# Performance work log

Measured on AMD Instinct MI355X. Metric: run time of the kernel, lower is better.

Reference implementation:

```python
import jax, jax.numpy as jnp
import numpy as np

D_MODEL = 2048
N_HEADS = 16
HEAD_DIM = D_MODEL // N_HEADS
D_FF = 8192


def setup_inputs() -> dict:
    key = jax.random.key(0)
    ks = jax.random.split(key, 16)
    s = 0.02
    inp = {
        'x': jax.random.normal(ks[0], (2, 2048, D_MODEL), dtype=jnp.float32),
        'Wq': jax.random.normal(ks[1], (D_MODEL, D_MODEL), jnp.float32) * s,
        'bq': jnp.zeros((D_MODEL,), jnp.float32),
        'Wk': jax.random.normal(ks[2], (D_MODEL, D_MODEL), jnp.float32) * s,
        'bk': jnp.zeros((D_MODEL,), jnp.float32),
        'Wv': jax.random.normal(ks[3], (D_MODEL, D_MODEL), jnp.float32) * s,
        'bv': jnp.zeros((D_MODEL,), jnp.float32),
        'Wo': jax.random.normal(ks[4], (D_MODEL, D_MODEL), jnp.float32) * s,
        'bo': jnp.zeros((D_MODEL,), jnp.float32),
        'rotary': jax.random.normal(ks[5], (1, 1, HEAD_DIM), jnp.float32) * s,
        'norm1_w': jnp.ones((D_MODEL,), jnp.float32),
        'norm2_w': jnp.ones((D_MODEL,), jnp.float32),
        'W1': jax.random.normal(ks[6], (2 * D_FF, D_MODEL), jnp.float32) * s,
        'b1': jnp.zeros((2 * D_FF,), jnp.float32),
        'W2': jax.random.normal(ks[7], (D_MODEL, D_FF), jnp.float32) * s,
        'b2': jnp.zeros((D_MODEL,), jnp.float32),
    }
    return inp


def _rmsnorm(x, w, eps=1e-8):
    return w * (x * jax.lax.rsqrt(jnp.mean(x * x, axis=-1, keepdims=True) + eps))


def reference(x, Wq, bq, Wk, bk, Wv, bv, Wo, bo, rotary, norm1_w, norm2_w, W1, b1, W2, b2):
    B, S, _ = x.shape
    # --- attention block ---
    h = _rmsnorm(x, norm1_w)
    q = (h @ Wq.T + bq).reshape(B, S, N_HEADS, HEAD_DIM)
    k = (h @ Wk.T + bk).reshape(B, S, N_HEADS, HEAD_DIM)
    v = (h @ Wv.T + bv).reshape(B, S, N_HEADS, HEAD_DIM)
    q = q + rotary  # (1,1,head_dim) broadcast over batch, seq, heads
    scores = jnp.einsum('bqhd,bkhd->bhqk', q, k) / jnp.sqrt(jnp.float32(HEAD_DIM))
    attn = jax.nn.softmax(scores, axis=-1)
    o = jnp.einsum('bhqk,bkhd->bqhd', attn, v).reshape(B, S, D_MODEL)
    x = x + (o @ Wo.T + bo)
    # --- SwiGLU FFN block ---
    h2 = _rmsnorm(x, norm2_w)
    g = h2 @ W1.T + b1
    x1, x2 = g[..., :D_FF], g[..., D_FF:]
    ff = (x1 * jax.nn.silu(x2)) @ W2.T + b2
    return x + ff
```

## Files before the change

### kernel.cpp

```cpp
#include <hip/hip_runtime.h>
#include <hip/hip_bf16.h>

#define D_MODEL 2048
#define N_HEADS 16
#define HEAD_DIM 128
#define D_FF 8192
#define BATCH 2
#define SEQ 2048
#define M_TOK (BATCH * SEQ)
#define QKV_LD 6144
#define QSCALE 0.12751744f

typedef __attribute__((ext_vector_type(8))) short short8;
typedef __attribute__((ext_vector_type(4))) short short4v;
typedef __attribute__((ext_vector_type(4))) float f32x4;
typedef __attribute__((ext_vector_type(16))) float f32x16;
typedef __attribute__((ext_vector_type(2))) unsigned int uint2v;
typedef __attribute__((ext_vector_type(4))) unsigned int uint4v;

__device__ __forceinline__ unsigned short f2b(float f) {
  __hip_bfloat16 h = __float2bfloat16(f);
  return *reinterpret_cast<unsigned short*>(&h);
}
__device__ __forceinline__ float b2f(unsigned short u) {
  unsigned int x = ((unsigned int)u) << 16;
  return __uint_as_float(x);
}

__device__ __forceinline__ void gload_lds16(const void* gsrc, void* ldst) {
  __builtin_amdgcn_global_load_lds(
      (const __attribute__((address_space(1))) void*)gsrc,
      (__attribute__((address_space(3))) void*)ldst, 16, 0, 0);
}

__device__ __forceinline__ f32x16 mfma32(short8 a, short8 b, f32x16 c) {
  return __builtin_amdgcn_mfma_f32_32x32x16_bf16(a, b, c, 0, 0, 0);
}
__device__ __forceinline__ unsigned int cvtpk(float lo, float hi) {
  unsigned int r;
  asm("v_cvt_pk_bf16_f32 %0, %1, %2" : "=v"(r) : "v"(lo), "v"(hi));
  return r;
}
__device__ __forceinline__ uint2v plswap(unsigned int a, unsigned int b) {
  return __builtin_amdgcn_permlane32_swap(a, b, false, false);
}

__global__ __launch_bounds__(256)
void cvt_all_kernel(const float* __restrict__ Wq, const float* __restrict__ Wk,
                    const float* __restrict__ Wv, const float* __restrict__ Wo,
                    const float* __restrict__ W2w,
                    unsigned short* __restrict__ wqkv,
                    unsigned short* __restrict__ wo,
                    unsigned short* __restrict__ w2) {
  const int NC = (D_MODEL * D_MODEL) / 8;
  const int TOT = 4 * NC + (D_MODEL * D_FF) / 8;
  int i = blockIdx.x * 256 + threadIdx.x;
  int stride = gridDim.x * 256;
  for (int c = i; c < TOT; c += stride) {
    const float* s;
    unsigned short* d;
    float sc = 1.0f;
    if (c < NC) { s = Wq + (size_t)c * 8; d = wqkv + (size_t)c * 8; sc = QSCALE; }
    else if (c < 2 * NC) { s = Wk + (size_t)(c - NC) * 8; d = wqkv + (size_t)c * 8; }
    else if (c < 3 * NC) { s = Wv + (size_t)(c - 2 * NC) * 8; d = wqkv + (size_t)c * 8; }
    else if (c < 4 * NC) { s = Wo + (size_t)(c - 3 * NC) * 8; d = wo + (size_t)(c - 3 * NC) * 8; }
    else { s = W2w + (size_t)(c - 4 * NC) * 8; d = w2 + (size_t)(c - 4 * NC) * 8; }
    const float4 a = *(const float4*)s;
    const float4 b = *(const float4*)(s + 4);
    short8 r;
    r[0] = f2b(a.x * sc); r[1] = f2b(a.y * sc);
    r[2] = f2b(a.z * sc); r[3] = f2b(a.w * sc);
    r[4] = f2b(b.x * sc); r[5] = f2b(b.y * sc);
    r[6] = f2b(b.z * sc); r[7] = f2b(b.w * sc);
    *(short8*)d = r;
  }
}

__global__ __launch_bounds__(256)
void cvt_w1p_kernel(const float* __restrict__ src,
                    unsigned short* __restrict__ dst) {
  int i = blockIdx.x * blockDim.x + threadIdx.x;
  int stride = gridDim.x * blockDim.x;
  const int total = 2 * D_FF * (D_MODEL / 8);
  for (int c = i; c < total; c += stride) {
    int rp = c >> 8, col8 = c & 255;
    int b = rp >> 6, half = (rp >> 5) & 1;
    int rs = half * D_FF + b * 32 + (rp & 31);
    const float* s = src + (size_t)rs * D_MODEL + col8 * 8;
    const float4 a = *(const float4*)s;
    const float4 bb = *(const float4*)(s + 4);
    short8 r;
    r[0] = f2b(a.x); r[1] = f2b(a.y); r[2] = f2b(a.z); r[3] = f2b(a.w);
    r[4] = f2b(bb.x); r[5] = f2b(bb.y); r[6] = f2b(bb.z); r[7] = f2b(bb.w);
    *(short8*)(dst + (size_t)c * 8) = r;
  }
}

__global__ void permb1_kernel(const float* __restrict__ b1,
                              float* __restrict__ b1p) {
  int i = blockIdx.x * 256 + threadIdx.x;
  int b = i >> 6, half = (i >> 5) & 1;
  b1p[i] = b1[half * D_FF + b * 32 + (i & 31)];
}

__global__ void biasqkv_kernel(const float* __restrict__ bq,
                               const float* __restrict__ bk,
                               const float* __restrict__ bv,
                               const float* __restrict__ rot,
                               float* __restrict__ outp) {
  int i = blockIdx.x * 256 + threadIdx.x;
  float v;
  if (i < 2048) v = (bq[i] + rot[i & (HEAD_DIM - 1)]) * QSCALE;
  else if (i < 4096) v = bk[i - 2048];
  else v = bv[i - 4096];
  outp[i] = v;
}

__global__ __launch_bounds__(256)
void rmsnorm_kernel(const float* __restrict__ x, const float* __restrict__ wv,
                    unsigned short* __restrict__ outp) {
  const int row = blockIdx.x;
  const float* xr = x + (size_t)row * D_MODEL;
  const int base = threadIdx.x * 8;
  float4 a = *(const float4*)(xr + base);
  float4 c = *(const float4*)(xr + base + 4);
  float ss = a.x * a.x + a.y * a.y + a.z * a.z + a.w * a.w +
             c.x * c.x + c.y * c.y + c.z * c.z + c.w * c.w;
#pragma unroll
  for (int m = 1; m < 64; m <<= 1) ss += __shfl_xor(ss, m);
  __shared__ float red[4];
  if ((threadIdx.x & 63) == 0) red[threadIdx.x >> 6] = ss;
  __syncthreads();
  float tot = red[0] + red[1] + red[2] + red[3];
  float sc = rsqrtf(tot * (1.0f / D_MODEL) + 1e-8f);
  float4 w0 = *(const float4*)(wv + base);
  float4 w1 = *(const float4*)(wv + base + 4);
  short8 r;
  r[0] = f2b(a.x * sc * w0.x); r[1] = f2b(a.y * sc * w0.y);
  r[2] = f2b(a.z * sc * w0.z); r[3] = f2b(a.w * sc * w0.w);
  r[4] = f2b(c.x * sc * w1.x); r[5] = f2b(c.y * sc * w1.y);
  r[6] = f2b(c.z * sc * w1.z); r[7] = f2b(c.w * sc * w1.w);
  *(short8*)(outp + (size_t)row * D_MODEL + base) = r;
}

template <int MODE>
__global__ __launch_bounds__(512, 2)
void gemm_p8(const unsigned short* __restrict__ A, int lda,
             const unsigned short* __restrict__ W, int ldw,
             const float* __restrict__ bias, void* __restrict__ outp,
             int N, int K, size_t out_zstride) {
  __shared__ unsigned short AL[2][2][128 * 64];
  __shared__ unsigned short BL[2][2][128 * 64];
  const int t = threadIdx.x;
  const int l = t & 63, w = t >> 6;
  const int wm = w >> 2, wn = w & 3;
  const int ln = l & 31, hi = l >> 5;
  const int m0 = blockIdx.y << 8, n0 = blockIdx.x << 8;
  const int koff = blockIdx.z * K;

  const int r0 = t >> 3;
  const int cb16 = (t & 7) * 16;
  const int sel = ((cb16 ^ ((r0 & 7) << 4)) >> 1);
  const unsigned short* Abase = A + (size_t)m0 * lda + koff;
  const unsigned short* Wbase = W + (size_t)n0 * ldw + koff;
  const int d0e = t * 8, d1e = (t + 512) * 8;

#define STAGE(XL, Xb, ld, dd, h, ktd)                                        \
  do {                                                                       \
    const unsigned short* s_ =                                               \
        (Xb) + (size_t)((h) * 128 + r0) * (ld) + (ktd) * 64 + sel;           \
    gload_lds16(s_, &XL[dd][h][d0e]);                                        \
    gload_lds16(s_ + (size_t)64 * (ld), &XL[dd][h][d1e]);                    \
  } while (0)

  const int swz = (ln & 7) << 4;
  const int hb = wn >> 1;
  const int browb = ((wn & 1) * 64 + ln) * 128;

  f32x16 acc[4][2] = {};
  short8 bf[2][4];

#define READB(dd)                                                            \
  do {                                                                       \
    const char* Bb_ = (const char*)&BL[dd][hb][0];                           \
    _Pragma("unroll") for (int cb_ = 0; cb_ < 2; cb_++)                      \
      _Pragma("unroll") for (int ks_ = 0; ks_ < 4; ks_++)                    \
        bf[cb_][ks_] = *(const short8*)(Bb_ + browb + cb_ * 4096 +           \
                                        ((ks_ * 32 + hi * 16) ^ swz));       \
  } while (0)

#define PHASE2(dd, p, STAGE_STMT, VM_STMT)                                   \
  do {                                                                       \
    const char* Ab_ = (const char*)&AL[dd][p][0];                            \
    short8 af_[2][4];                                                        \
    if ((p) == 0) READB(dd);                                                 \
    _Pragma("unroll") for (int sb_ = 0; sb_ < 2; sb_++) {                    \
      _Pragma("unroll") for (int ks_ = 0; ks_ < 4; ks_++)                    \
        af_[sb_][ks_] = *(const short8*)(Ab_ +                               \
                                         (wm * 64 + sb_ * 32 + ln) * 128 +   \
                                         ((ks_ * 32 + hi * 16) ^ swz));      \
    }                                                                        \
    STAGE_STMT;                                                              \
    __builtin_amdgcn_sched_barrier(0);                                       \
    VM_STMT;                                                                 \
    __builtin_amdgcn_sched_barrier(0);                                       \
    __builtin_amdgcn_s_barrier();                                            \
    __builtin_amdgcn_sched_barrier(0);                                       \
    __builtin_amdgcn_s_setprio(1);                                           \
    _Pragma("unroll") for (int sb_ = 0; sb_ < 2; sb_++)                      \
      _Pragma("unroll") for (int cb_ = 0; cb_ < 2; cb_++)                    \
        _Pragma("unroll") for (int ks_ = 0; ks_ < 4; ks_++)                  \
          acc[2 * (p) + sb_][cb_] =                                          \
              mfma32(af_[sb_][ks_], bf[cb_][ks_], acc[2 * (p) + sb_][cb_]);  \
    __builtin_amdgcn_s_setprio(0);                                           \
    __builtin_amdgcn_sched_barrier(0);                                       \
    __builtin_amdgcn_s_barrier();                                            \
    __builtin_amdgcn_sched_barrier(0);                                       \
  } while (0)

  const int NT = K >> 6;

  STAGE(AL, Abase, lda, 0, 0, 0);
  STAGE(AL, Abase, lda, 0, 1, 0);
  STAGE(BL, Wbase, ldw, 0, 0, 0);
  STAGE(BL, Wbase, ldw, 0, 1, 0);
  STAGE(AL, Abase, lda, 1, 0, 1);
  STAGE(BL, Wbase, ldw, 1, 0, 1);
  asm volatile("s_waitcnt vmcnt(4)" ::: "memory");
  __builtin_amdgcn_sched_barrier(0);
  __builtin_amdgcn_s_barrier();
  __builtin_amdgcn_sched_barrier(0);

  for (int kt = 0; kt < NT; kt += 2) {
    PHASE2(0, 0,
           {
             if (kt + 1 < NT) {
               STAGE(BL, Wbase, ldw, 1, 1, kt + 1);
               STAGE(AL, Abase, lda, 1, 1, kt + 1);
             }
           },
           {});
    PHASE2(0, 1,
           {
             if (kt + 2 < NT) {
               STAGE(AL, Abase, lda, 0, 0, kt + 2);
               STAGE(BL, Wbase, ldw, 0, 0, kt + 2);
             }
           },
           {
             if (kt + 2 < NT)
               asm volatile("s_waitcnt vmcnt(4)" ::: "memory");
             else
               asm volatile("s_waitcnt vmcnt(0)" ::: "memory");
           });
    PHASE2(1, 0,
           {
             if (kt + 2 < NT) {
               STAGE(BL, Wbase, ldw, 0, 1, kt + 2);
               STAGE(AL, Abase, lda, 0, 1, kt + 2);
             }
           },
           {});
    PHASE2(1, 1,
           {
             if (kt + 3 < NT) {
               STAGE(AL, Abase, lda, 1, 0, kt + 3);
               STAGE(BL, Wbase, ldw, 1, 0, kt + 3);
             }
           },
           {
             if (kt + 3 < NT)
               asm volatile("s_waitcnt vmcnt(4)" ::: "memory");
             else
               asm volatile("s_waitcnt vmcnt(0)" ::: "memory");
           });
  }
#undef PHASE2
#undef READB
#undef STAGE

#pragma unroll
  for (int rb = 0; rb < 4; rb++) {
    const int rowb = m0 + (rb >> 1) * 128 + wm * 64 + (rb & 1) * 32 + 4 * hi;
    if (MODE == 3) {
      const int col0 = n0 + wn * 64 + ln;
      const float b1v = bias[col0];
      const float b2v = bias[col0 + 32];
      const int jout = (n0 >> 1) + wn * 32 + ln;
#pragma unroll
      for (int r = 0; r < 16; r++) {
        const int row = rowb + (r & 3) + 8 * (r >> 2);
        float x1 = acc[rb][0][r] + b1v;
        float x2 = acc[rb][1][r] + b2v;
        float sg = x2 * __builtin_amdgcn_rcpf(1.0f + __expf(-x2));
        ((unsigned short*)outp)[(size_t)row * (N >> 1) + jout] = f2b(x1 * sg);
      }
    } else {
#pragma unroll
      for (int cb = 0; cb < 2; cb++) {
        const int col = n0 + wn * 64 + cb * 32 + ln;
        const float bv = (MODE == 0) ? bias[col] : 0.0f;
#pragma unroll
        for (int r = 0; r < 16; r++) {
          const int row = rowb + (r & 3) + 8 * (r >> 2);
          const float vv = acc[rb][cb][r] + bv;
          if (MODE == 0)
            ((unsigned short*)outp)[(size_t)row * N + col] = f2b(vv);
          else
            ((unsigned short*)outp + blockIdx.z * out_zstride)
                [(size_t)row * N + col] = f2b(vv);
        }
      }
    }
  }
}

__global__ __launch_bounds__(256)
void vtrans_kernel(const unsigned short* __restrict__ qkv,
                   unsigned short* __restrict__ vt) {
  const int bh = blockIdx.y;
  const int b = bh >> 4, h = bh & 15;
  const int s0 = blockIdx.x * 32;
  __shared__ unsigned short tile[32][136];
  const int t = threadIdx.x;
  for (int i = 0; i < 2; i++) {
    int c = t + i * 256;
    int s = c >> 4, dc = c & 15;
    *(short8*)&tile[s][dc * 8] =
        *(const short8*)(qkv + (size_t)(b * SEQ + s0 + s) * QKV_LD + 4096 +
                         h * HEAD_DIM + dc * 8);
  }
  __syncthreads();
  const int d = t >> 1, sh = (t & 1) * 16;
  unsigned short* dst = vt + ((size_t)bh * HEAD_DIM + d) * SEQ + s0 + sh;
  short8 r0, r1;
#pragma unroll
  for (int j = 0; j < 8; j++) r0[j] = tile[sh + j][d];
#pragma unroll
  for (int j = 0; j < 8; j++) r1[j] = tile[sh + 8 + j][d];
  *(short8*)dst = r0;
  *(short8*)(dst + 8) = r1;
}

__global__ __launch_bounds__(512, 2)
void attn_kernel(const unsigned short* __restrict__ qkv,
                 const unsigned short* __restrict__ vt,
                 unsigned short* __restrict__ o) {
  const int bh = blockIdx.y;
  const int b = bh >> 4, h = bh & 15;
  const int q0 = blockIdx.x << 8;
  const int t = threadIdx.x, w = t >> 6, l = t & 63;
  const int ln = l & 31, hi = l >> 5;

  __shared__ unsigned short Ks[2][64 * 128];

  short8 qf[8];
  {
    const unsigned short* qb =
        qkv + (size_t)(b * SEQ + q0 + w * 32 + ln) * QKV_LD + h * HEAD_DIM +
        hi * 8;
#pragma unroll
    for (int sl = 0; sl < 8; sl++) qf[sl] = *(const short8*)(qb + sl * 16);
  }

  f32x16 oacc[4] = {};
  float mrow = -1e30f, lrow = 0.f;

  const unsigned short* kbase =
      qkv + (size_t)(b * SEQ) * QKV_LD + 2048 + h * HEAD_DIM;
  const unsigned short* vbase = vt + (size_t)bh * HEAD_DIM * SEQ;

#define STAGEK(buf, kv0_)                                                    \
  do {                                                                       \
    _Pragma("unroll") for (int i_ = 0; i_ < 2; i_++) {                       \
      int c_ = t + i_ * 512;                                                 \
      int row_ = c_ >> 4, dc_ = c_ & 15;                                     \
      int sel_ = ((dc_ * 16) ^ ((row_ & 7) << 4)) >> 1;                      \
      gload_lds16(kbase + (size_t)((kv0_) + row_) * QKV_LD + sel_,           \
                  &Ks[buf][c_ * 8]);                                         \
    }                                                                        \
  } while (0)

  STAGEK(0, 0);
  __syncthreads();

  for (int it = 0; it < SEQ / 64; ++it) {
    const int cur = it & 1;
    const int kv0 = it * 64;

    short8 vf[4][4];
#pragma unroll
    for (int db = 0; db < 4; db++)
#pragma unroll
      for (int ks = 0; ks < 4; ks++)
        vf[db][ks] = *(const short8*)(vbase + (size_t)(db * 32 + ln) * SEQ +
                                      kv0 + ks * 16 + hi * 8);

    if (it + 1 < SEQ / 64) STAGEK(cur ^ 1, kv0 + 64);

    const char* kb = (const char*)&Ks[cur][0];
    f32x16 s0 = {}, s1 = {};
    __builtin_amdgcn_s_setprio(1);
#pragma unroll
    for (int sl = 0; sl < 8; sl++) {
      const int cw = (sl * 32 + hi * 16) ^ ((ln & 7) << 4);
      short8 kf0 = *(const short8*)(kb + ln * 256 + cw);
      short8 kf1 = *(const short8*)(kb + (32 + ln) * 256 + cw);
      s0 = mfma32(kf0, qf[sl], s0);
      s1 = mfma32(kf1, qf[sl], s1);
    }
    __builtin_amdgcn_s_setprio(0);

    float mx = s0[0];
#pragma unroll
    for (int r = 1; r < 16; r++) mx = fmaxf(mx, s0[r]);
#pragma unroll
    for (int r = 0; r < 16; r++) mx = fmaxf(mx, s1[r]);
    {
      uint2v r2 = plswap(__float_as_uint(mx), __float_as_uint(mx));
      mx = fmaxf(__uint_as_float(r2[0]), __uint_as_float(r2[1]));
    }

    if (!__all(mx <= mrow + 8.f)) {
      float mnew = fmaxf(mrow, mx);
      float fs = exp2f(mrow - mnew);
      mrow = mnew;
      lrow *= fs;
#pragma unroll
      for (int db = 0; db < 4; db++)
#pragma unroll
        for (int r = 0; r < 16; r++) oacc[db][r] *= fs;
    }

    float p0[16], p1[16];
    float sum = 0.f;
#pragma unroll
    for (int r = 0; r < 16; r++) {
      p0[r] = exp2f(s0[r] - mrow);
      sum += p0[r];
    }
#pragma unroll
    for (int r = 0; r < 16; r++) {
      p1[r] = exp2f(s1[r] - mrow);
      sum += p1[r];
    }
    lrow += sum;

    uint4v pk[4];
#define PACKSUB(P, K0)                                                       \
  {                                                                          \
    unsigned int a_, b_;                                                     \
    uint2v r_;                                                               \
    a_ = cvtpk(P[0], P[1]); b_ = cvtpk(P[4], P[5]);                          \
    r_ = plswap(a_, b_); pk[K0][0] = r_[0]; pk[K0][2] = r_[1];               \
    a_ = cvtpk(P[2], P[3]); b_ = cvtpk(P[6], P[7]);                          \
    r_ = plswap(a_, b_); pk[K0][1] = r_[0]; pk[K0][3] = r_[1];               \
    a_ = cvtpk(P[8], P[9]); b_ = cvtpk(P[12], P[13]);                        \
    r_ = plswap(a_, b_); pk[K0 + 1][0] = r_[0]; pk[K0 + 1][2] = r_[1];       \
    a_ = cvtpk(P[10], P[11]); b_ = cvtpk(P[14], P[15]);                      \
    r_ = plswap(a_, b_); pk[K0 + 1][1] = r_[0]; pk[K0 + 1][3] = r_[1];       \
  }
    PACKSUB(p0, 0);
    PACKSUB(p1, 2);
#undef PACKSUB

    __builtin_amdgcn_s_setprio(1);
#pragma unroll
    for (int db = 0; db < 4; db++)
#pragma unroll
      for (int ks = 0; ks < 4; ks++)
        oacc[db] = mfma32(vf[db][ks], __builtin_bit_cast(short8, pk[ks]),
                          oacc[db]);
    __builtin_amdgcn_s_setprio(0);

    __syncthreads();
  }
#undef STAGEK

  {
    uint2v r2 = plswap(__float_as_uint(lrow), __float_as_uint(lrow));
    lrow = __uint_as_float(r2[0]) + __uint_as_float(r2[1]);
  }
  const float inv = 1.0f / lrow;
  unsigned short* ob = o + (size_t)(b * SEQ + q0 + w * 32 + ln) * D_MODEL +
                       h * HEAD_DIM + hi * 4;
#pragma unroll
  for (int db = 0; db < 4; db++)
#pragma unroll
    for (int r = 0; r < 4; r++) {
      short4v v4;
#pragma unroll
      for (int j = 0; j < 4; j++)
        v4[j] = (short)f2b(oacc[db][4 * r + j] * inv);
      *(short4v*)(ob + db * 32 + r * 8) = v4;
    }
}

__global__ __launch_bounds__(256)
void reduceo_norm_kernel(const unsigned short* __restrict__ p0,
                         const unsigned short* __restrict__ p1,
                         const float* __restrict__ bo,
                         const float* __restrict__ x,
                         const float* __restrict__ n2w,
                         float* __restrict__ out,
                         unsigned short* __restrict__ h2) {
  const int row = blockIdx.x;
  const int base = threadIdx.x * 8;
  const size_t off = (size_t)row * D_MODEL + base;
  short8 a = *(const short8*)(p0 + off);
  short8 b = *(const short8*)(p1 + off);
  float4 x0 = *(const float4*)(x + off);
  float4 x1 = *(const float4*)(x + off + 4);
  float4 bo0 = *(const float4*)(bo + base);
  float4 bo1 = *(const float4*)(bo + base + 4);
  float o[8];
  o[0] = b2f((unsigned short)a[0]) + b2f((unsigned short)b[0]) + x0.x + bo0.x;
  o[1] = b2f((unsigned short)a[1]) + b2f((unsigned short)b[1]) + x0.y + bo0.y;
  o[2] = b2f((unsigned short)a[2]) + b2f((unsigned short)b[2]) + x0.z + bo0.z;
  o[3] = b2f((unsigned short)a[3]) + b2f((unsigned short)b[3]) + x0.w + bo0.w;
  o[4] = b2f((unsigned short)a[4]) + b2f((unsigned short)b[4]) + x1.x + bo1.x;
  o[5] = b2f((unsigned short)a[5]) + b2f((unsigned short)b[5]) + x1.y + bo1.y;
  o[6] = b2f((unsigned short)a[6]) + b2f((unsigned short)b[6]) + x1.z + bo1.z;
  o[7] = b2f((unsigned short)a[7]) + b2f((unsigned short)b[7]) + x1.w + bo1.w;
  float4 w0, w1;
  w0.x = o[0]; w0.y = o[1]; w0.z = o[2]; w0.w = o[3];
  w1.x = o[4]; w1.y = o[5]; w1.z = o[6]; w1.w = o[7];
  *(float4*)(out + off) = w0;
  *(float4*)(out + off + 4) = w1;
  float ss = 0.f;
#pragma unroll
  for (int j = 0; j < 8; j++) ss += o[j] * o[j];
#pragma unroll
  for (int m = 1; m < 64; m <<= 1) ss += __shfl_xor(ss, m);
  __shared__ float red[4];
  if ((threadIdx.x & 63) == 0) red[threadIdx.x >> 6] = ss;
  __syncthreads();
  float tot = red[0] + red[1] + red[2] + red[3];
  float sc = rsqrtf(tot * (1.0f / D_MODEL) + 1e-8f);
  float4 g0 = *(const float4*)(n2w + base);
  float4 g1 = *(const float4*)(n2w + base + 4);
  short8 r;
  r[0] = f2b(o[0] * sc * g0.x); r[1] = f2b(o[1] * sc * g0.y);
  r[2] = f2b(o[2] * sc * g0.z); r[3] = f2b(o[3] * sc * g0.w);
  r[4] = f2b(o[4] * sc * g1.x); r[5] = f2b(o[5] * sc * g1.y);
  r[6] = f2b(o[6] * sc * g1.z); r[7] = f2b(o[7] * sc * g1.w);
  *(short8*)(h2 + off) = r;
}

__global__ __launch_bounds__(256)
void reduce2_kernel(const unsigned short* __restrict__ p0,
                    const unsigned short* __restrict__ p1,
                    const float* __restrict__ b2, float* __restrict__ out) {
  size_t i = (size_t)blockIdx.x * 256 + threadIdx.x;
  const int col8 = (int)(i & 255) * 8;
  short8 a = *(const short8*)(p0 + i * 8);
  short8 b = *(const short8*)(p1 + i * 8);
  float4 o0 = ((const float4*)out)[i * 2];
  float4 o1 = ((const float4*)out)[i * 2 + 1];
  float4 bb0 = *(const float4*)(b2 + col8);
  float4 bb1 = *(const float4*)(b2 + col8 + 4);
  o0.x += b2f((unsigned short)a[0]) + b2f((unsigned short)b[0]) + bb0.x;
  o0.y += b2f((unsigned short)a[1]) + b2f((unsigned short)b[1]) + bb0.y;
  o0.z += b2f((unsigned short)a[2]) + b2f((unsigned short)b[2]) + bb0.z;
  o0.w += b2f((unsigned short)a[3]) + b2f((unsigned short)b[3]) + bb0.w;
  o1.x += b2f((unsigned short)a[4]) + b2f((unsigned short)b[4]) + bb1.x;
  o1.y += b2f((unsigned short)a[5]) + b2f((unsigned short)b[5]) + bb1.y;
  o1.z += b2f((unsigned short)a[6]) + b2f((unsigned short)b[6]) + bb1.z;
  o1.w += b2f((unsigned short)a[7]) + b2f((unsigned short)b[7]) + bb1.w;
  ((float4*)out)[i * 2] = o0;
  ((float4*)out)[i * 2 + 1] = o1;
}

extern "C" void kernel_launch(void* const* d_in, const int* in_sizes, int n_in,
                              void* d_out, int out_size, void* d_ws,
                              size_t ws_size, hipStream_t stream) {
  (void)in_sizes; (void)n_in; (void)out_size; (void)ws_size;
  const float* x   = (const float*)d_in[0];
  const float* Wq  = (const float*)d_in[1];
  const float* bq  = (const float*)d_in[2];
  const float* Wk  = (const float*)d_in[3];
  const float* bk  = (const float*)d_in[4];
  const float* Wv  = (const float*)d_in[5];
  const float* bv  = (const float*)d_in[6];
  const float* Wo  = (const float*)d_in[7];
  const float* bo  = (const float*)d_in[8];
  const float* rot = (const float*)d_in[9];
  const float* n1w = (const float*)d_in[10];
  const float* n2w = (const float*)d_in[11];
  const float* W1  = (const float*)d_in[12];
  const float* b1  = (const float*)d_in[13];
  const float* W2  = (const float*)d_in[14];
  const float* b2  = (const float*)d_in[15];
  float* out = (float*)d_out;
  char* ws = (char*)d_ws;

  const size_t SZ_D2  = (size_t)D_MODEL * D_MODEL * 2;
  const size_t SZ_ACT = (size_t)M_TOK * D_MODEL * 2;
  const size_t SZ_W1  = (size_t)2 * D_FF * D_MODEL * 2;
  const size_t SZ_W2  = (size_t)D_MODEL * D_FF * 2;
  const size_t SZ_G   = (size_t)M_TOK * 2 * D_FF * 2;

  size_t off = 0;
  auto alloc = [&](size_t sz) { size_t o = off; off += (sz + 255) & ~(size_t)255; return o; };
  unsigned short* wqkv_b = (unsigned short*)(ws + alloc(3 * SZ_D2));
  unsigned short* wo_b   = (unsigned short*)(ws + alloc(SZ_D2));
  unsigned short* w1_b   = (unsigned short*)(ws + alloc(SZ_W1));
  unsigned short* w2_b   = (unsigned short*)(ws + alloc(SZ_W2));
  float*          biasq  = (float*)(ws + alloc(QKV_LD * 4));
  float*          b1p    = (float*)(ws + alloc(2 * D_FF * 4));
  unsigned short* h2_b   = (unsigned short*)(ws + alloc(SZ_ACT));
  char* pool = ws + alloc(SZ_G);
  unsigned short* h_b   = (unsigned short*)(pool);
  unsigned short* qkv_b = (unsigned short*)(pool + SZ_ACT);
  unsigned short* vt_b  = (unsigned short*)(pool + 4 * SZ_ACT);
  unsigned short* o_b   = (unsigned short*)(pool + 5 * SZ_ACT);
  unsigned short* po0 = (unsigned short*)pool;
  unsigned short* po1 = po0 + (size_t)M_TOK * D_MODEL;
  unsigned short* ff_b  = (unsigned short*)(pool);
  unsigned short* p0 = (unsigned short*)ws;
  unsigned short* p1 = p0 + (size_t)M_TOK * D_MODEL;

  cvt_all_kernel<<<2048, 256, 0, stream>>>(Wq, Wk, Wv, Wo, W2, wqkv_b, wo_b, w2_b);
  cvt_w1p_kernel<<<2048, 256, 0, stream>>>(W1, w1_b);
  biasqkv_kernel<<<QKV_LD / 256, 256, 0, stream>>>(bq, bk, bv, rot, biasq);
  permb1_kernel<<<2 * D_FF / 256, 256, 0, stream>>>(b1, b1p);

  rmsnorm_kernel<<<M_TOK, 256, 0, stream>>>(x, n1w, h_b);

  gemm_p8<0><<<dim3(QKV_LD / 256, M_TOK / 256), 512, 0, stream>>>(
      h_b, D_MODEL, wqkv_b, D_MODEL, biasq, qkv_b, QKV_LD, D_MODEL, 0);

  vtrans_kernel<<<dim3(SEQ / 32, BATCH * N_HEADS), 256, 0, stream>>>(qkv_b, vt_b);
  attn_kernel<<<dim3(SEQ / 256, BATCH * N_HEADS), 512, 0, stream>>>(qkv_b, vt_b, o_b);

  gemm_p8<2><<<dim3(D_MODEL / 256, M_TOK / 256, 2), 512, 0, stream>>>(
      o_b, D_MODEL, wo_b, D_MODEL, nullptr, po0, D_MODEL, D_MODEL / 2,
      (size_t)M_TOK * D_MODEL);
  reduceo_norm_kernel<<<M_TOK, 256, 0, stream>>>(po0, po1, bo, x, n2w, out, h2_b);

  gemm_p8<3><<<dim3(2 * D_FF / 256, M_TOK / 256), 512, 0, stream>>>(
      h2_b, D_MODEL, w1_b, D_MODEL, b1p, ff_b, 2 * D_FF, D_MODEL, 0);

  gemm_p8<2><<<dim3(D_MODEL / 256, M_TOK / 256, 2), 512, 0, stream>>>(
      ff_b, D_FF, w2_b, D_FF, nullptr, p0, D_MODEL, D_FF / 2,
      (size_t)M_TOK * D_MODEL);

  reduce2_kernel<<<(M_TOK * D_MODEL / 8) / 256, 256, 0, stream>>>(p0, p1, b2, out);
}
```

Baseline: 852.0 us.

## Merge weight-conversion and bias kernels; deepen attention K staging to four buffers

The W1 permute-convert pass is folded into the shared weight conversion kernel, and the QKV bias and b1 permutation kernels are merged into one, so fewer launches run. The attention kernel goes from two to four LDS K buffers and processes two 64-key tiles per barrier, prefetching the next 128 keys ahead. This halves the block-wide syncs in the attention loop and gives K loads more time to arrive, at the cost of doubled LDS use, which may limit residency of the 512-thread, two-block-per-CU configuration.

After: 854.1 us. No clear change (+0.2%).

```diff
diff --git a/kernel.cpp b/kernel.cpp
--- a/kernel.cpp
+++ b/kernel.cpp
@@ -48,12 +48,15 @@
 __global__ __launch_bounds__(256)
 void cvt_all_kernel(const float* __restrict__ Wq, const float* __restrict__ Wk,
                     const float* __restrict__ Wv, const float* __restrict__ Wo,
-                    const float* __restrict__ W2w,
+                    const float* __restrict__ W2w, const float* __restrict__ W1w,
                     unsigned short* __restrict__ wqkv,
                     unsigned short* __restrict__ wo,
-                    unsigned short* __restrict__ w2) {
+                    unsigned short* __restrict__ w2,
+                    unsigned short* __restrict__ w1p) {
   const int NC = (D_MODEL * D_MODEL) / 8;
-  const int TOT = 4 * NC + (D_MODEL * D_FF) / 8;
+  const int NW2 = (D_MODEL * D_FF) / 8;
+  const int NW1 = (2 * D_FF * D_MODEL) / 8;
+  const int TOT = 4 * NC + NW2 + NW1;
   int i = blockIdx.x * 256 + threadIdx.x;
   int stride = gridDim.x * 256;
   for (int c = i; c < TOT; c += stride) {
@@ -64,7 +67,15 @@
     else if (c < 2 * NC) { s = Wk + (size_t)(c - NC) * 8; d = wqkv + (size_t)c * 8; }
     else if (c < 3 * NC) { s = Wv + (size_t)(c - 2 * NC) * 8; d = wqkv + (size_t)c * 8; }
     else if (c < 4 * NC) { s = Wo + (size_t)(c - 3 * NC) * 8; d = wo + (size_t)(c - 3 * NC) * 8; }
-    else { s = W2w + (size_t)(c - 4 * NC) * 8; d = w2 + (size_t)(c - 4 * NC) * 8; }
+    else if (c < 4 * NC + NW2) { s = W2w + (size_t)(c - 4 * NC) * 8; d = w2 + (size_t)(c - 4 * NC) * 8; }
+    else {
+      int cc = c - 4 * NC - NW2;
+      int rp = cc >> 8, col8 = cc & 255;
+      int b = rp >> 6, half = (rp >> 5) & 1;
+      int rs = half * D_FF + b * 32 + (rp & 31);
+      s = W1w + (size_t)rs * D_MODEL + col8 * 8;
+      d = w1p + (size_t)cc * 8;
+    }
     const float4 a = *(const float4*)s;
     const float4 b = *(const float4*)(s + 4);
     short8 r;
@@ -76,44 +87,25 @@
   }
 }
 
-__global__ __launch_bounds__(256)
-void cvt_w1p_kernel(const float* __restrict__ src,
-                    unsigned short* __restrict__ dst) {
-  int i = blockIdx.x * blockDim.x + threadIdx.x;
-  int stride = gridDim.x * blockDim.x;
-  const int total = 2 * D_FF * (D_MODEL / 8);
-  for (int c = i; c < total; c += stride) {
-    int rp = c >> 8, col8 = c & 255;
-    int b = rp >> 6, half = (rp >> 5) & 1;
-    int rs = half * D_FF + b * 32 + (rp & 31);
-    const float* s = src + (size_t)rs * D_MODEL + col8 * 8;
-    const float4 a = *(const float4*)s;
-    const float4 bb = *(const float4*)(s + 4);
-    short8 r;
-    r[0] = f2b(a.x); r[1] = f2b(a.y); r[2] = f2b(a.z); r[3] = f2b(a.w);
-    r[4] = f2b(bb.x); r[5] = f2b(bb.y); r[6] = f2b(bb.z); r[7] = f2b(bb.w);
-    *(short8*)(dst + (size_t)c * 8) = r;
-  }
-}
-
-__global__ void permb1_kernel(const float* __restrict__ b1,
-                              float* __restrict__ b1p) {
+__global__ void bias_kernel(const float* __restrict__ bq,
+                            const float* __restrict__ bk,
+                            const float* __restrict__ bv,
+                            const float* __restrict__ rot,
+                            const float* __restrict__ b1,
+                            float* __restrict__ biasq,
+                            float* __restrict__ b1p) {
   int i = blockIdx.x * 256 + threadIdx.x;
-  int b = i >> 6, half = (i >> 5) & 1;
-  b1p[i] = b1[half * D_FF + b * 32 + (i & 31)];
-}
-
-__global__ void biasqkv_kernel(const float* __restrict__ bq,
-                               const float* __restrict__ bk,
-                               const float* __restrict__ bv,
-                               const float* __restrict__ rot,
-                               float* __restrict__ outp) {
-  int i = blockIdx.x * 256 + threadIdx.x;
-  float v;
-  if (i < 2048) v = (bq[i] + rot[i & (HEAD_DIM - 1)]) * QSCALE;
-  else if (i < 4096) v = bk[i - 2048];
-  else v = bv[i - 4096];
-  outp[i] = v;
+  if (i < QKV_LD) {
+    float v;
+    if (i < 2048) v = (bq[i] + rot[i & (HEAD_DIM - 1)]) * QSCALE;
+    else if (i < 4096) v = bk[i - 2048];
+    else v = bv[i - 4096];
+    biasq[i] = v;
+  } else {
+    int j = i - QKV_LD;
+    int b = j >> 6, half = (j >> 5) & 1;
+    b1p[j] = b1[half * D_FF + b * 32 + (j & 31)];
+  }
 }
 
 __global__ __launch_bounds__(256)
@@ -352,7 +344,7 @@
   const int t = threadIdx.x, w = t >> 6, l = t & 63;
   const int ln = l & 31, hi = l >> 5;
 
-  __shared__ unsigned short Ks[2][64 * 128];
+  __shared__ unsigned short Ks[4][64 * 128];
 
   short8 qf[8];
   {
@@ -381,100 +373,95 @@
     }                                                                        \
   } while (0)
 
+#define PROC_TILE(buf, kv0_)                                                 \
+  do {                                                                       \
+    short8 vf[4][4];                                                         \
+    _Pragma("unroll") for (int db = 0; db < 4; db++)                         \
+      _Pragma("unroll") for (int ks = 0; ks < 4; ks++)                       \
+        vf[db][ks] = *(const short8*)(vbase + (size_t)(db * 32 + ln) * SEQ + \
+                                      (kv0_) + ks * 16 + hi * 8);            \
+    const char* kb = (const char*)&Ks[buf][0];                               \
+    f32x16 s0 = {}, s1 = {};                                                 \
+    __builtin_amdgcn_s_setprio(1);                                           \
+    _Pragma("unroll") for (int sl = 0; sl < 8; sl++) {                       \
+      const int cw = (sl * 32 + hi * 16) ^ ((ln & 7) << 4);                  \
+      short8 kf0 = *(const short8*)(kb + ln * 256 + cw);                     \
+      short8 kf1 = *(const short8*)(kb + (32 + ln) * 256 + cw);              \
+      s0 = mfma32(kf0, qf[sl], s0);                                          \
+      s1 = mfma32(kf1, qf[sl], s1);                                          \
+    }                                                                        \
+    __builtin_amdgcn_s_setprio(0);                                           \
+    float mx = s0[0];                                                        \
+    _Pragma("unroll") for (int r = 1; r < 16; r++) mx = fmaxf(mx, s0[r]);    \
+    _Pragma("unroll") for (int r = 0; r < 16; r++) mx = fmaxf(mx, s1[r]);    \
+    {                                                                        \
+      uint2v r2 = plswap(__float_as_uint(mx), __float_as_uint(mx));          \
+      mx = fmaxf(__uint_as_float(r2[0]), __uint_as_float(r2[1]));            \
+    }                                                                        \
+    if (!__all(mx <= mrow + 8.f)) {                                          \
+      float mnew = fmaxf(mrow, mx);                                          \
+      float fs = exp2f(mrow - mnew);                                         \
+      mrow = mnew;                                                           \
+      lrow *= fs;                                                            \
+      _Pragma("unroll") for (int db = 0; db < 4; db++)                       \
+        _Pragma("unroll") for (int r = 0; r < 16; r++) oacc[db][r] *= fs;    \
+    }                                                                        \
+    float p0[16], p1[16];                                                    \
+    float sum = 0.f;                                                         \
+    _Pragma("unroll") for (int r = 0; r < 16; r++) {                         \
+      p0[r] = exp2f(s0[r] - mrow);                                           \
+      sum += p0[r];                                                          \
+    }                                                                        \
+    _Pragma("unroll") for (int r = 0; r < 16; r++) {                         \
+      p1[r] = exp2f(s1[r] - mrow);                                           \
+      sum += p1[r];                                                          \
+    }                                                                        \
+    lrow += sum;                                                             \
+    uint4v pk[4];                                                            \
+    {                                                                        \
+      unsigned int a_, b_;                                                   \
+      uint2v r_;                                                             \
+      a_ = cvtpk(p0[0], p0[1]); b_ = cvtpk(p0[4], p0[5]);                    \
+      r_ = plswap(a_, b_); pk[0][0] = r_[0]; pk[0][2] = r_[1];               \
+      a_ = cvtpk(p0[2], p0[3]); b_ = cvtpk(p0[6], p0[7]);                    \
+      r_ = plswap(a_, b_); pk[0][1] = r_[0]; pk[0][3] = r_[1];               \
+      a_ = cvtpk(p0[8], p0[9]); b_ = cvtpk(p0[12], p0[13]);                  \
+      r_ = plswap(a_, b_); pk[1][0] = r_[0]; pk[1][2] = r_[1];               \
+      a_ = cvtpk(p0[10], p0[11]); b_ = cvtpk(p0[14], p0[15]);                \
+      r_ = plswap(a_, b_); pk[1][1] = r_[0]; pk[1][3] = r_[1];               \
+      a_ = cvtpk(p1[0], p1[1]); b_ = cvtpk(p1[4], p1[5]);                    \
+      r_ = plswap(a_, b_); pk[2][0] = r_[0]; pk[2][2] = r_[1];               \
+      a_ = cvtpk(p1[2], p1[3]); b_ = cvtpk(p1[6], p1[7]);                    \
+      r_ = plswap(a_, b_); pk[2][1] = r_[0]; pk[2][3] = r_[1];               \
+      a_ = cvtpk(p1[8], p1[9]); b_ = cvtpk(p1[12], p1[13]);                  \
+      r_ = plswap(a_, b_); pk[3][0] = r_[0]; pk[3][2] = r_[1];               \
+      a_ = cvtpk(p1[10], p1[11]); b_ = cvtpk(p1[14], p1[15]);                \
+      r_ = plswap(a_, b_); pk[3][1] = r_[0]; pk[3][3] = r_[1];               \
+    }                                                                        \
+    __builtin_amdgcn_s_setprio(1);                                           \
+    _Pragma("unroll") for (int db = 0; db < 4; db++)                         \
+      _Pragma("unroll") for (int ks = 0; ks < 4; ks++)                       \
+        oacc[db] = mfma32(vf[db][ks], __builtin_bit_cast(short8, pk[ks]),    \
+                          oacc[db]);                                         \
+    __builtin_amdgcn_s_setprio(0);                                           \
+  } while (0)
+
   STAGEK(0, 0);
+  STAGEK(1, 64);
   __syncthreads();
 
-  for (int it = 0; it < SEQ / 64; ++it) {
-    const int cur = it & 1;
-    const int kv0 = it * 64;
-
-    short8 vf[4][4];
-#pragma unroll
-    for (int db = 0; db < 4; db++)
-#pragma unroll
-      for (int ks = 0; ks < 4; ks++)
-        vf[db][ks] = *(const short8*)(vbase + (size_t)(db * 32 + ln) * SEQ +
-                                      kv0 + ks * 16 + hi * 8);
-
-    if (it + 1 < SEQ / 64) STAGEK(cur ^ 1, kv0 + 64);
-
-    const char* kb = (const char*)&Ks[cur][0];
-    f32x16 s0 = {}, s1 = {};
-    __builtin_amdgcn_s_setprio(1);
-#pragma unroll
-    for (int sl = 0; sl < 8; sl++) {
-      const int cw = (sl * 32 + hi * 16) ^ ((ln & 7) << 4);
-      short8 kf0 = *(const short8*)(kb + ln * 256 + cw);
-      short8 kf1 = *(const short8*)(kb + (32 + ln) * 256 + cw);
-      s0 = mfma32(kf0, qf[sl], s0);
-      s1 = mfma32(kf1, qf[sl], s1);
+  for (int w2 = 0; w2 < SEQ / 128; ++w2) {
+    const int kv0 = w2 * 128;
+    const int ba = (2 * w2) & 3, bb = (2 * w2 + 1) & 3;
+    if (w2 + 1 < SEQ / 128) {
+      STAGEK((2 * w2 + 2) & 3, kv0 + 128);
+      STAGEK((2 * w2 + 3) & 3, kv0 + 192);
     }
-    __builtin_amdgcn_s_setprio(0);
-
-    float mx = s0[0];
-#pragma unroll
-    for (int r = 1; r < 16; r++) mx = fmaxf(mx, s0[r]);
-#pragma unroll
-    for (int r = 0; r < 16; r++) mx = fmaxf(mx, s1[r]);
-    {
-      uint2v r2 = plswap(__float_as_uint(mx), __float_as_uint(mx));
-      mx = fmaxf(__uint_as_float(r2[0]), __uint_as_float(r2[1]));
-    }
-
-    if (!__all(mx <= mrow + 8.f)) {
-      float mnew = fmaxf(mrow, mx);
-      float fs = exp2f(mrow - mnew);
-      mrow = mnew;
-      lrow *= fs;
-#pragma unroll
-      for (int db = 0; db < 4; db++)
-#pragma unroll
-        for (int r = 0; r < 16; r++) oacc[db][r] *= fs;
-    }
-
-    float p0[16], p1[16];
-    float sum = 0.f;
-#pragma unroll
-    for (int r = 0; r < 16; r++) {
-      p0[r] = exp2f(s0[r] - mrow);
-      sum += p0[r];
-    }
-#pragma unroll
-    for (int r = 0; r < 16; r++) {
-      p1[r] = exp2f(s1[r] - mrow);
-      sum += p1[r];
-    }
-    lrow += sum;
-
-    uint4v pk[4];
-#define PACKSUB(P, K0)                                                       \
-  {                                                                          \
-    unsigned int a_, b_;                                                     \
-    uint2v r_;                                                               \
-    a_ = cvtpk(P[0], P[1]); b_ = cvtpk(P[4], P[5]);                          \
-    r_ = plswap(a_, b_); pk[K0][0] = r_[0]; pk[K0][2] = r_[1];               \
-    a_ = cvtpk(P[2], P[3]); b_ = cvtpk(P[6], P[7]);                          \
-    r_ = plswap(a_, b_); pk[K0][1] = r_[0]; pk[K0][3] = r_[1];               \
-    a_ = cvtpk(P[8], P[9]); b_ = cvtpk(P[12], P[13]);                        \
-    r_ = plswap(a_, b_); pk[K0 + 1][0] = r_[0]; pk[K0 + 1][2] = r_[1];       \
-    a_ = cvtpk(P[10], P[11]); b_ = cvtpk(P[14], P[15]);                      \
-    r_ = plswap(a_, b_); pk[K0 + 1][1] = r_[0]; pk[K0 + 1][3] = r_[1];       \
-  }
-    PACKSUB(p0, 0);
-    PACKSUB(p1, 2);
-#undef PACKSUB
-
-    __builtin_amdgcn_s_setprio(1);
-#pragma unroll
-    for (int db = 0; db < 4; db++)
-#pragma unroll
-      for (int ks = 0; ks < 4; ks++)
-        oacc[db] = mfma32(vf[db][ks], __builtin_bit_cast(short8, pk[ks]),
-                          oacc[db]);
-    __builtin_amdgcn_s_setprio(0);
-
+    PROC_TILE(ba, kv0);
+    PROC_TILE(bb, kv0 + 64);
     __syncthreads();
   }
+#undef PROC_TILE
 #undef STAGEK
 
   {
@@ -620,10 +607,10 @@
   unsigned short* p0 = (unsigned short*)ws;
   unsigned short* p1 = p0 + (size_t)M_TOK * D_MODEL;
 
-  cvt_all_kernel<<<2048, 256, 0, stream>>>(Wq, Wk, Wv, Wo, W2, wqkv_b, wo_b, w2_b);
-  cvt_w1p_kernel<<<2048, 256, 0, stream>>>(W1, w1_b);
-  biasqkv_kernel<<<QKV_LD / 256, 256, 0, stream>>>(bq, bk, bv, rot, biasq);
-  permb1_kernel<<<2 * D_FF / 256, 256, 0, stream>>>(b1, b1p);
+  cvt_all_kernel<<<2048, 256, 0, stream>>>(Wq, Wk, Wv, Wo, W2, W1,
+                                           wqkv_b, wo_b, w2_b, w1_b);
+  bias_kernel<<<(QKV_LD + 2 * D_FF) / 256, 256, 0, stream>>>(
+      bq, bk, bv, rot, b1, biasq, b1p);
 
   rmsnorm_kernel<<<M_TOK, 256, 0, stream>>>(x, n1w, h_b);
 
```
